# Kernel optimization log

Hardware: AMD Instinct MI355X
Metric: run time of the kernel (lower is better)

The kernel has to match this reference:

```python
import jax, jax.numpy as jnp
import numpy as np

PATCH = 16  # patch_size

def _patchify(images, p=PATCH):
    # images: [B, H, W] -> patches: [B, N, p*p] in raster order
    B, H, W = images.shape
    x = images.reshape(B, H // p, p, W // p, p)
    x = x.transpose(0, 1, 3, 2, 4)  # [B, H/p, W/p, p, p]
    return x.reshape(B, (H // p) * (W // p), p * p)

def setup_inputs() -> dict:
    key = jax.random.key(0)
    k1, k2 = jax.random.split(key)
    images = jax.random.normal(k1, (64, 256, 256), dtype=jnp.float32)
    vocab = jax.random.normal(k2, (4096, 256), dtype=jnp.float32)  # [V, patch^2]
    return {"images": images, "vocab": vocab}

def reference(images, vocab):
    # forward_patches: patchify (raster ordering -> identity permutation)
    patches = _patchify(images)  # [B, N, D]
    # forward_tokens: torch.cdist + argmin. argmin of Euclidean distance
    # equals argmin of squared distance; expand ||x-v||^2 to avoid the
    # explicit [B, N, V, D] difference tensor.
    v2 = jnp.sum(vocab * vocab, axis=-1)                      # [V]
    xv = jnp.einsum('bnd,vd->bnv', patches, vocab)            # [B, N, V]
    x2 = jnp.sum(patches * patches, axis=-1, keepdims=True)   # [B, N, 1]
    d2 = x2 - 2.0 * xv + v2                                   # [B, N, V]
    tokens = jnp.argmin(d2, axis=-1)                          # [B, N] int
    return patches, tokens
```

## Files before the change

kernel.cpp:

```cpp
#include <hip/hip_runtime.h>
#include <math.h>

#define PS      16
#define D       256
#define V       4096
#define M       16384
#define NSPLIT  64
#define PAIR_CAP 1048576
#define QMARGIN 130

typedef _Float16 half8 __attribute__((ext_vector_type(8)));
typedef _Float16 half4 __attribute__((ext_vector_type(4)));
typedef float    f32x4 __attribute__((ext_vector_type(4)));

__device__ __forceinline__ void gload_lds16(const void* g, void* l) {
  __builtin_amdgcn_global_load_lds(
      (const __attribute__((address_space(1))) unsigned int*)g,
      (__attribute__((address_space(3))) unsigned int*)l, 16, 0, 0);
}

__global__ __launch_bounds__(256) void prep_kernel(
    const float* __restrict__ img, const float* __restrict__ vocab,
    float* __restrict__ outp, _Float16* __restrict__ Ah,
    _Float16* __restrict__ Vh, float* __restrict__ v2,
    int* __restrict__ paircount) {
  if (blockIdx.x < 4096) {
    if (blockIdx.x == 0 && threadIdx.x == 0) *paircount = 0;
    const int t  = blockIdx.x * 256 + threadIdx.x;
    const int o4 = t << 2;
    const int b   = o4 >> 16;
    const int rem = o4 & 65535;
    const int n   = rem >> 8;
    const int d   = rem & 255;
    const int py = n >> 4, px = n & 15, i = d >> 4, j = d & 15;
    const float4 v = *(const float4*)(img + (b << 16) + ((py * PS + i) << 8) + px * PS + j);
    *(float4*)(outp + o4) = v;
    half4 h = { (_Float16)v.x, (_Float16)v.y, (_Float16)v.z, (_Float16)v.w };
    *(half4*)(Ah + o4) = h;
  } else {
    const int gtid = (blockIdx.x - 4096) * 256 + threadIdx.x;
    const int row  = gtid >> 6;
    const int lane = gtid & 63;
    const float4 v = *(const float4*)(vocab + (size_t)row * D + (lane << 2));
    half4 h = { (_Float16)v.x, (_Float16)v.y, (_Float16)v.z, (_Float16)v.w };
    *(half4*)(Vh + (size_t)row * D + (lane << 2)) = h;
    float s = v.x * v.x + v.y * v.y + v.z * v.z + v.w * v.w;
    #pragma unroll
    for (int off = 32; off > 0; off >>= 1) s += __shfl_down(s, off);
    if (lane == 0) v2[row] = s;
  }
}

__global__ __launch_bounds__(256, 3) void gemm_score_kernel(
    const _Float16* __restrict__ Ah,
    const _Float16* __restrict__ Vh,
    const float* __restrict__ v2,
    unsigned* __restrict__ pk1, unsigned* __restrict__ pk2) {
  __shared__ __align__(16) _Float16 Af[8 * 64 * 32];

  const int tid  = threadIdx.x;
  const int lane = tid & 63;
  const int wid  = tid >> 6;
  const int row0 = blockIdx.x * 64;
  const int sp   = blockIdx.y;
  const int col0 = sp * 256 + wid * 64;
  const int grp  = sp * 4 + wid;

  {
    const int srow = lane >> 2;
    const int sg   = ((lane & 3) ^ ((srow >> 1) & 3)) << 3;
    const _Float16* Ag = Ah + (size_t)(row0 + wid * 16 + srow) * D + sg;
    _Float16* Al = Af + wid * 16 * 32;
    #pragma unroll
    for (int kt = 0; kt < 8; ++kt)
      gload_lds16(Ag + kt * 32, Al + kt * 64 * 32);
  }
  __syncthreads();

  const int cl = lane & 15;
  const int q  = lane >> 4;
  const int fg = (q ^ ((cl >> 1) & 3)) << 3;
  const _Float16* Ab = Af + cl * 32 + fg;
  const _Float16* Bp = Vh + (size_t)(col0 + cl) * D + q * 8;

  f32x4 acc[4][4];
  #pragma unroll
  for (int i = 0; i < 4; ++i)
    #pragma unroll
    for (int j = 0; j < 4; ++j) acc[i][j] = (f32x4){0.f, 0.f, 0.f, 0.f};

  half8 bn[4], afn[4];
  #pragma unroll
  for (int j = 0; j < 4; ++j) bn[j] = *(const half8*)(Bp + (size_t)j * 16 * D);
  #pragma unroll
  for (int i = 0; i < 4; ++i) afn[i] = *(const half8*)(Ab + i * 512);

  #pragma unroll 1
  for (int kt = 0; kt < 8; ++kt) {
    half8 b[4], af[4];
    #pragma unroll
    for (int j = 0; j < 4; ++j) b[j] = bn[j];
    #pragma unroll
    for (int i = 0; i < 4; ++i) af[i] = afn[i];
    if (kt < 7) {
      #pragma unroll
      for (int j = 0; j < 4; ++j)
        bn[j] = *(const half8*)(Bp + (size_t)j * 16 * D + (kt + 1) * 32);
      #pragma unroll
      for (int i = 0; i < 4; ++i)
        afn[i] = *(const half8*)(Ab + (kt + 1) * 2048 + i * 512);
    }
    #pragma unroll
    for (int i = 0; i < 4; ++i)
      #pragma unroll
      for (int j = 0; j < 4; ++j)
        acc[i][j] = __builtin_amdgcn_mfma_f32_16x16x32_f16(af[i], b[j], acc[i][j], 0, 0, 0);
  }

  float Cj[4];
  #pragma unroll
  for (int j = 0; j < 4; ++j) Cj[j] = fmaf(v2[col0 + j * 16 + cl], 512.0f, 524288.0f);
  unsigned kk1[16], kk2[16];
  #pragma unroll
  for (int i = 0; i < 4; ++i)
    #pragma unroll
    for (int r = 0; r < 4; ++r) {
      const int p = i * 4 + r;
      unsigned K1 = 0xFFFFFFFFu, K2 = 0xFFFFFFFFu;
      #pragma unroll
      for (int j = 0; j < 4; ++j) {
        const unsigned key =
            ((unsigned)fmaf(-1024.0f, acc[i][j][r], Cj[j]) << 12) |
            (unsigned)(col0 + j * 16 + cl);
        K2 = min(K2, max(K1, key));
        K1 = min(K1, key);
      }
      kk1[p] = K1; kk2[p] = K2;
    }
  #pragma unroll
  for (int p = 0; p < 16; ++p) {
    unsigned k1 = kk1[p], k2 = kk2[p];
    #pragma unroll
    for (int mask = 1; mask <= 8; mask <<= 1) {
      const unsigned o1 = (unsigned)__shfl_xor((int)k1, mask);
      const unsigned o2 = (unsigned)__shfl_xor((int)k2, mask);
      k2 = min(min(k2, o2), max(k1, o1));
      k1 = min(k1, o1);
    }
    kk1[p] = k1; kk2[p] = k2;
  }
  if (cl == 0) {
    #pragma unroll
    for (int p = 0; p < 16; ++p) {
      const int rl = (p >> 2) * 16 + q * 4 + (p & 3);
      pk1[(size_t)grp * M + row0 + rl] = kk1[p];
      pk2[(size_t)grp * M + row0 + rl] = kk2[p];
    }
  }
}

__global__ __launch_bounds__(256) void reduce_gather_kernel(
    const unsigned* __restrict__ pk1, const unsigned* __restrict__ pk2,
    float* __restrict__ tok, unsigned long long* __restrict__ minkey,
    unsigned* __restrict__ pairs, int* __restrict__ paircount) {
  const int m = blockIdx.x * 256 + threadIdx.x;
  unsigned K1 = 0xFFFFFFFFu, K2 = 0xFFFFFFFFu;
  for (int s = 0; s < NSPLIT; ++s) {
    const unsigned b1 = pk1[(size_t)s * M + m];
    const unsigned b2 = pk2[(size_t)s * M + m];
    K2 = min(min(K2, b2), max(K1, b1));
    K1 = min(K1, b1);
  }
  tok[m] = (float)(K1 & 4095u);
  minkey[m] = 0xFFFFFFFFFFFFFFFFull;
  if ((int)(K2 >> 12) - (int)(K1 >> 12) <= QMARGIN) {
    const int th = (int)(K1 >> 12) + QMARGIN;
    int cnt = 0;
    for (int s = 0; s < NSPLIT; ++s) {
      const unsigned b1 = pk1[(size_t)s * M + m];
      const unsigned b2 = pk2[(size_t)s * M + m];
      cnt += ((int)(b2 >> 12) <= th) ? 64
           : (((int)(b1 >> 12) <= th) ? 1 : 0);
    }
    int base = atomicAdd(paircount, cnt);
    if (base + cnt <= PAIR_CAP) {
      const unsigned mh = (unsigned)m << 12;
      for (int s = 0; s < NSPLIT; ++s) {
        const unsigned b1 = pk1[(size_t)s * M + m];
        const unsigned b2 = pk2[(size_t)s * M + m];
        if ((int)(b2 >> 12) <= th) {
          for (int r = 0; r < 64; ++r) pairs[base + r] = mh | (unsigned)(s * 64 + r);
          base += 64;
        } else if ((int)(b1 >> 12) <= th) {
          pairs[base++] = mh | (b1 & 4095u);
        }
      }
    }
  }
}

__global__ __launch_bounds__(256) void refine_score(
    const float* __restrict__ patches, const float* __restrict__ vocab,
    const unsigned* __restrict__ pairs, const int* __restrict__ paircount,
    unsigned long long* __restrict__ minkey) {
  const int lane = threadIdx.x & 63;
  const int gw = (blockIdx.x * 256 + threadIdx.x) >> 6;
  const int nw = (gridDim.x * 256) >> 6;
  int np = *paircount;
  if (np > PAIR_CAP) np = PAIR_CAP;
  for (int i = gw; i < np; i += nw) {
    const unsigned pr = pairs[i];
    const int m = pr >> 12, row = pr & 4095;
    const float4 pv = *(const float4*)(patches + (size_t)m * D + (lane << 2));
    const float4 vv = *(const float4*)(vocab + (size_t)row * D + (lane << 2));
    double acc = 0.0, df;
    df = (double)pv.x - (double)vv.x; acc = fma(df, df, acc);
    df = (double)pv.y - (double)vv.y; acc = fma(df, df, acc);
    df = (double)pv.z - (double)vv.z; acc = fma(df, df, acc);
    df = (double)pv.w - (double)vv.w; acc = fma(df, df, acc);
    #pragma unroll
    for (int off = 32; off > 0; off >>= 1) acc += __shfl_down(acc, off);
    if (lane == 0) {
      const unsigned long long key =
          ((unsigned long long)__double_as_longlong(acc) & ~0xFFFull) | (unsigned)row;
      atomicMin(&minkey[m], key);
    }
  }
}

__global__ __launch_bounds__(256) void refine_final(
    const unsigned* __restrict__ pairs, const int* __restrict__ paircount,
    const unsigned long long* __restrict__ minkey, float* __restrict__ tok) {
  int np = *paircount;
  if (np > PAIR_CAP) np = PAIR_CAP;
  for (int i = blockIdx.x * 256 + threadIdx.x; i < np; i += gridDim.x * 256) {
    const int m = pairs[i] >> 12;
    tok[m] = (float)(unsigned)(minkey[m] & 4095ull);
  }
}

extern "C" void kernel_launch(void* const* d_in, const int* in_sizes, int n_in,
                              void* d_out, int out_size, void* d_ws, size_t ws_size,
                              hipStream_t stream) {
  const float* images = (const float*)d_in[0];
  const float* vocab  = (const float*)d_in[1];
  float* out     = (float*)d_out;
  float* patches = out;
  float* tokens  = out + (size_t)M * D;

  char* ws = (char*)d_ws;
  _Float16* Ah       = (_Float16*)(ws);
  _Float16* Vh       = (_Float16*)(ws + 8388608);
  float*    v2       = (float*)   (ws + 10485760);
  unsigned* pk1      = (unsigned*)(ws + 10502144);
  unsigned* pk2      = (unsigned*)(ws + 14696448);
  unsigned long long* minkey = (unsigned long long*)(ws + 18890752);
  int*      paircount= (int*)     (ws + 19021824);
  unsigned* pairs    = (unsigned*)(ws + 19021888);

  prep_kernel<<<4096 + 1024, 256, 0, stream>>>(images, vocab, patches, Ah,
                                               Vh, v2, paircount);
  gemm_score_kernel<<<dim3(M / 64, V / 256), 256, 0, stream>>>(Ah, Vh, v2, pk1, pk2);
  reduce_gather_kernel<<<M / 256, 256, 0, stream>>>(pk1, pk2, tokens, minkey,
                                                    pairs, paircount);
  refine_score<<<512, 256, 0, stream>>>(patches, vocab, pairs, paircount, minkey);
  refine_final<<<64, 256, 0, stream>>>(pairs, paircount, minkey, tokens);
}
```

Baseline: 185.8 us.

## Pre-swizzle fp16 operands into MFMA fragment layout, drop register prefetch

The prep kernel now writes the fp16 patch and vocab matrices in a tiled layout that matches the MFMA 16x16x32 fragment order. The GEMM then loads A as contiguous LDS chunks without XOR swizzle, and loads B fragments as coalesced 16-byte reads. The explicit register double-buffer prefetch is removed, which lowers register pressure so the launch bound can ask for 4 waves per SIMD instead of 3. The trade-off is that load latency is now hidden only by occupancy rather than by software prefetch.

```diff
diff --git a/kernel.cpp b/kernel.cpp
--- a/kernel.cpp
+++ b/kernel.cpp
@@ -19,41 +19,47 @@
       (__attribute__((address_space(3))) unsigned int*)l, 16, 0, 0);
 }
 
+
 __global__ __launch_bounds__(256) void prep_kernel(
     const float* __restrict__ img, const float* __restrict__ vocab,
-    float* __restrict__ outp, _Float16* __restrict__ Ah,
-    _Float16* __restrict__ Vh, float* __restrict__ v2,
+    float* __restrict__ outp, _Float16* __restrict__ Ah2,
+    _Float16* __restrict__ Vh2, float* __restrict__ v2,
     int* __restrict__ paircount) {
   if (blockIdx.x < 4096) {
     if (blockIdx.x == 0 && threadIdx.x == 0) *paircount = 0;
     const int t  = blockIdx.x * 256 + threadIdx.x;
     const int o4 = t << 2;
-    const int b   = o4 >> 16;
-    const int rem = o4 & 65535;
-    const int n   = rem >> 8;
-    const int d   = rem & 255;
+    const int m   = o4 >> 8;
+    const int d   = o4 & 255;
+    const int b   = m >> 8;
+    const int n   = m & 255;
     const int py = n >> 4, px = n & 15, i = d >> 4, j = d & 15;
     const float4 v = *(const float4*)(img + (b << 16) + ((py * PS + i) << 8) + px * PS + j);
     *(float4*)(outp + o4) = v;
     half4 h = { (_Float16)v.x, (_Float16)v.y, (_Float16)v.z, (_Float16)v.w };
-    *(half4*)(Ah + o4) = h;
+    const int fa = (m >> 6) * 16384 + (d >> 5) * 2048 + ((m >> 4) & 3) * 512 +
+                   ((d >> 3) & 3) * 128 + (m & 15) * 8 + (d & 7);
+    *(half4*)(Ah2 + fa) = h;
   } else {
     const int gtid = (blockIdx.x - 4096) * 256 + threadIdx.x;
-    const int row  = gtid >> 6;
+    const int c    = gtid >> 6;
     const int lane = gtid & 63;
-    const float4 v = *(const float4*)(vocab + (size_t)row * D + (lane << 2));
+    const int d0   = lane << 2;
+    const float4 v = *(const float4*)(vocab + (size_t)c * D + d0);
     half4 h = { (_Float16)v.x, (_Float16)v.y, (_Float16)v.z, (_Float16)v.w };
-    *(half4*)(Vh + (size_t)row * D + (lane << 2)) = h;
+    const int fv = (c >> 8) * 65536 + (d0 >> 5) * 8192 + ((c >> 4) & 15) * 512 +
+                   ((d0 >> 3) & 3) * 128 + (c & 15) * 8 + (d0 & 7);
+    *(half4*)(Vh2 + fv) = h;
     float s = v.x * v.x + v.y * v.y + v.z * v.z + v.w * v.w;
     #pragma unroll
     for (int off = 32; off > 0; off >>= 1) s += __shfl_down(s, off);
-    if (lane == 0) v2[row] = s;
-  }
-}
-
-__global__ __launch_bounds__(256, 3) void gemm_score_kernel(
-    const _Float16* __restrict__ Ah,
-    const _Float16* __restrict__ Vh,
+    if (lane == 0) v2[c] = s;
+  }
+}
+
+__global__ __launch_bounds__(256, 4) void gemm_score_kernel(
+    const _Float16* __restrict__ Ah2,
+    const _Float16* __restrict__ Vh2,
     const float* __restrict__ v2,
     unsigned* __restrict__ pk1, unsigned* __restrict__ pk2) {
   __shared__ __align__(16) _Float16 Af[8 * 64 * 32];
@@ -61,55 +67,40 @@
   const int tid  = threadIdx.x;
   const int lane = tid & 63;
   const int wid  = tid >> 6;
-  const int row0 = blockIdx.x * 64;
-  const int sp   = blockIdx.y;
+  const int rowblk = blockIdx.x;
+  const int sp     = blockIdx.y;
+  const int row0 = rowblk * 64;
   const int col0 = sp * 256 + wid * 64;
   const int grp  = sp * 4 + wid;
 
   {
-    const int srow = lane >> 2;
-    const int sg   = ((lane & 3) ^ ((srow >> 1) & 3)) << 3;
-    const _Float16* Ag = Ah + (size_t)(row0 + wid * 16 + srow) * D + sg;
-    _Float16* Al = Af + wid * 16 * 32;
-    #pragma unroll
-    for (int kt = 0; kt < 8; ++kt)
-      gload_lds16(Ag + kt * 32, Al + kt * 64 * 32);
+    const _Float16* src = Ah2 + (size_t)rowblk * 16384 + wid * 4096 + lane * 8;
+    _Float16* dst = Af + wid * 4096;
+    #pragma unroll
+    for (int t = 0; t < 8; ++t)
+      gload_lds16(src + t * 512, dst + t * 512);
   }
   __syncthreads();
 
   const int cl = lane & 15;
   const int q  = lane >> 4;
-  const int fg = (q ^ ((cl >> 1) & 3)) << 3;
-  const _Float16* Ab = Af + cl * 32 + fg;
-  const _Float16* Bp = Vh + (size_t)(col0 + cl) * D + q * 8;
+  const _Float16* Ak = Af + q * 128 + cl * 8;
+  const _Float16* Bk = Vh2 + (size_t)sp * 65536 + wid * 2048 + q * 128 + cl * 8;
 
   f32x4 acc[4][4];
   #pragma unroll
   for (int i = 0; i < 4; ++i)
     #pragma unroll
     for (int j = 0; j < 4; ++j) acc[i][j] = (f32x4){0.f, 0.f, 0.f, 0.f};
-
-  half8 bn[4], afn[4];
-  #pragma unroll
-  for (int j = 0; j < 4; ++j) bn[j] = *(const half8*)(Bp + (size_t)j * 16 * D);
-  #pragma unroll
-  for (int i = 0; i < 4; ++i) afn[i] = *(const half8*)(Ab + i * 512);
 
   #pragma unroll 1
   for (int kt = 0; kt < 8; ++kt) {
     half8 b[4], af[4];
     #pragma unroll
-    for (int j = 0; j < 4; ++j) b[j] = bn[j];
-    #pragma unroll
-    for (int i = 0; i < 4; ++i) af[i] = afn[i];
-    if (kt < 7) {
-      #pragma unroll
-      for (int j = 0; j < 4; ++j)
-        bn[j] = *(const half8*)(Bp + (size_t)j * 16 * D + (kt + 1) * 32);
-      #pragma unroll
-      for (int i = 0; i < 4; ++i)
-        afn[i] = *(const half8*)(Ab + (kt + 1) * 2048 + i * 512);
-    }
+    for (int j = 0; j < 4; ++j) b[j] = *(const half8*)(Bk + j * 512);
+    #pragma unroll
+    for (int i = 0; i < 4; ++i) af[i] = *(const half8*)(Ak + i * 512);
+    Bk += 8192; Ak += 2048;
     #pragma unroll
     for (int i = 0; i < 4; ++i)
       #pragma unroll
@@ -249,8 +240,8 @@
   float* tokens  = out + (size_t)M * D;
 
   char* ws = (char*)d_ws;
-  _Float16* Ah       = (_Float16*)(ws);
-  _Float16* Vh       = (_Float16*)(ws + 8388608);
+  _Float16* Ah2      = (_Float16*)(ws);
+  _Float16* Vh2      = (_Float16*)(ws + 8388608);
   float*    v2       = (float*)   (ws + 10485760);
   unsigned* pk1      = (unsigned*)(ws + 10502144);
   unsigned* pk2      = (unsigned*)(ws + 14696448);
@@ -258,9 +249,9 @@
   int*      paircount= (int*)     (ws + 19021824);
   unsigned* pairs    = (unsigned*)(ws + 19021888);
 
-  prep_kernel<<<4096 + 1024, 256, 0, stream>>>(images, vocab, patches, Ah,
-                                               Vh, v2, paircount);
-  gemm_score_kernel<<<dim3(M / 64, V / 256), 256, 0, stream>>>(Ah, Vh, v2, pk1, pk2);
+  prep_kernel<<<4096 + 1024, 256, 0, stream>>>(images, vocab, patches, Ah2,
+                                               Vh2, v2, paircount);
+  gemm_score_kernel<<<dim3(M / 64, V / 256), 256, 0, stream>>>(Ah2, Vh2, v2, pk1, pk2);
   reduce_gather_kernel<<<M / 256, 256, 0, stream>>>(pk1, pk2, tokens, minkey,
                                                     pairs, paircount);
   refine_score<<<512, 256, 0, stream>>>(patches, vocab, pairs, paircount, minkey);
```

Result: faster. 163.6 us (-12.0%).
